# Kernel optimization log

Measured on AMD Instinct MI355X. Metric: run time of the kernel, lower is better.

## Reference

```python
import jax, jax.numpy as jnp
import numpy as np

DIM = 2048
N_HEADS = 16
N_KV_HEADS = 4
HEAD_DIM = DIM // N_HEADS  # 128
N_REP = N_HEADS // N_KV_HEADS
MAX_SEQ_LEN = 4096
SEQLEN = 4096


def setup_inputs() -> dict:
    key = jax.random.key(0)
    ks = jax.random.split(key, 6)
    x = jax.random.normal(ks[0], (1, SEQLEN, DIM), dtype=jnp.float32)
    # rotary frequencies, llama-style theta=10000
    inv_freq = 1.0 / (10000.0 ** (np.arange(0, HEAD_DIM, 2, dtype=np.float32) / HEAD_DIM))
    t = np.arange(SEQLEN, dtype=np.float32)
    ang = np.outer(t, inv_freq)  # [S, head_dim/2]
    freqs_cos = jnp.asarray(np.cos(ang))
    freqs_sin = jnp.asarray(np.sin(ang))
    # additive causal mask [S, S]
    mask = jnp.where(jnp.tril(jnp.ones((SEQLEN, SEQLEN), dtype=bool)), 0.0, -1e9).astype(jnp.float32)
    sc = 0.02
    wq = jax.random.normal(ks[1], (DIM, N_HEADS * HEAD_DIM), dtype=jnp.float32) * sc
    wk = jax.random.normal(ks[2], (DIM, N_KV_HEADS * HEAD_DIM), dtype=jnp.float32) * sc
    wv = jax.random.normal(ks[3], (DIM, N_KV_HEADS * HEAD_DIM), dtype=jnp.float32) * sc
    wo = jax.random.normal(ks[4], (N_HEADS * HEAD_DIM, DIM), dtype=jnp.float32) * sc
    return {"x": x, "start_pos": 0, "freqs_cos": freqs_cos, "freqs_sin": freqs_sin,
            "mask": mask, "wq": wq, "wk": wk, "wv": wv, "wo": wo}


def _rope(x, cos, sin):
    # x: [b, s, h, d]; cos/sin: [s, d/2]; consecutive pairs form complex numbers
    b, s, h, d = x.shape
    xr = x.astype(jnp.float32).reshape(b, s, h, d // 2, 2)
    x1, x2 = xr[..., 0], xr[..., 1]
    c = cos[None, :, None, :]
    sn = sin[None, :, None, :]
    o1 = x1 * c - x2 * sn
    o2 = x1 * sn + x2 * c
    return jnp.stack([o1, o2], axis=-1).reshape(b, s, h, d).astype(x.dtype)


def reference(x, start_pos, freqs_cos, freqs_sin, mask, wq, wk, wv, wo):
    bsz, seqlen, _ = x.shape
    xq = (x @ wq).reshape(bsz, seqlen, N_HEADS, HEAD_DIM)
    xk = (x @ wk).reshape(bsz, seqlen, N_KV_HEADS, HEAD_DIM)
    xv = (x @ wv).reshape(bsz, seqlen, N_KV_HEADS, HEAD_DIM)
    xq = _rope(xq, freqs_cos, freqs_sin)
    xk = _rope(xk, freqs_cos, freqs_sin)
    # KV-cache append (cache is zeros before this call)
    cache_k = jnp.zeros((1, MAX_SEQ_LEN, N_KV_HEADS, HEAD_DIM), dtype=xk.dtype)
    cache_v = jnp.zeros((1, MAX_SEQ_LEN, N_KV_HEADS, HEAD_DIM), dtype=xv.dtype)
    cache_k = jax.lax.dynamic_update_slice(cache_k, xk, (0, start_pos, 0, 0))
    cache_v = jax.lax.dynamic_update_slice(cache_v, xv, (0, start_pos, 0, 0))
    keys = cache_k[:bsz, : start_pos + seqlen]    # [b, T, kvh, d]
    values = cache_v[:bsz, : start_pos + seqlen]
    # GQA repeat to full head count
    keys = jnp.repeat(keys, N_REP, axis=2)
    values = jnp.repeat(values, N_REP, axis=2)
    scale = 1.0 / jnp.sqrt(jnp.float32(HEAD_DIM))
    scores = jnp.einsum('bshd,bthd->bhst', xq, keys) * scale  # [b, h, s, T]
    scores = scores + mask[None, None, :, :]
    probs = jax.nn.softmax(scores.astype(jnp.float32), axis=-1).astype(xq.dtype)
    out = jnp.einsum('bhst,bthd->bshd', probs, values).reshape(bsz, seqlen, -1)
    return out @ wo
```

## Files before the change

kernel.cpp:

```cpp
#include <hip/hip_runtime.h>
#include <hip/hip_bf16.h>
#include <stdint.h>

#define SEQ 4096
#define DIM 2048
#define NH 16
#define NKV 4
#define HD 128
#define KVLD 1024


using frag8 = __attribute__((ext_vector_type(8))) short;
using f32x4 = __attribute__((ext_vector_type(4))) float;

union VecU { ushort u[8]; uint4 v; };

__device__ __forceinline__ float bf2f(ushort u) {
    union { uint32_t u; float f; } v; v.u = ((uint32_t)u) << 16; return v.f;
}
__device__ __forceinline__ ushort f2bf(float f) {
    union { float f; uint32_t u; } v; v.f = f;
    uint32_t r = v.u + 0x7fffu + ((v.u >> 16) & 1u);
    return (ushort)(r >> 16);
}

__device__ __forceinline__ void glds16(const void* g, void* l) {
    __builtin_amdgcn_global_load_lds(
        (const __attribute__((address_space(1))) void*)g,
        (__attribute__((address_space(3))) void*)l, 16, 0, 0);
}

__global__ __launch_bounds__(256) void cvt_kernel(
    const float* __restrict__ src, ushort* __restrict__ dst)
{
    size_t i = ((size_t)blockIdx.x * 256 + threadIdx.x) * 8;
    float4 f0 = *(const float4*)&src[i];
    float4 f1 = *(const float4*)&src[i + 4];
    VecU t;
    t.u[0] = f2bf(f0.x); t.u[1] = f2bf(f0.y); t.u[2] = f2bf(f0.z); t.u[3] = f2bf(f0.w);
    t.u[4] = f2bf(f1.x); t.u[5] = f2bf(f1.y); t.u[6] = f2bf(f1.z); t.u[7] = f2bf(f1.w);
    *(uint4*)&dst[i] = t.v;
}

__global__ __launch_bounds__(256) void convT_kernel(
    const float* __restrict__ src, ushort* __restrict__ dst, int K, int N)
{
    __shared__ ushort T[32][36];
    int r  = threadIdx.x >> 3;
    int c4 = (threadIdx.x & 7) * 4;
    int bk = blockIdx.y * 32, bn = blockIdx.x * 32;
    float4 v = *(const float4*)&src[(size_t)(bk + r) * N + bn + c4];
    T[r][c4]     = f2bf(v.x); T[r][c4 + 1] = f2bf(v.y);
    T[r][c4 + 2] = f2bf(v.z); T[r][c4 + 3] = f2bf(v.w);
    __syncthreads();
    ushort4 o;
    o.x = T[c4][r]; o.y = T[c4 + 1][r]; o.z = T[c4 + 2][r]; o.w = T[c4 + 3][r];
    *(ushort4*)&dst[(size_t)(bn + r) * K + bk + c4] = o;
}

__global__ __launch_bounds__(256) void vtrans_kernel(
    const ushort* __restrict__ src, ushort* __restrict__ dst)
{
    __shared__ ushort T[32][36];
    int r  = threadIdx.x >> 3;
    int c4 = (threadIdx.x & 7) * 4;
    int bt = blockIdx.y * 32, bd = blockIdx.x * 32;
    ushort4 v = *(const ushort4*)&src[(size_t)(bt + r) * KVLD + 512 + bd + c4];
    T[r][c4] = v.x; T[r][c4 + 1] = v.y; T[r][c4 + 2] = v.z; T[r][c4 + 3] = v.w;
    __syncthreads();
    ushort4 o;
    o.x = T[c4][r]; o.y = T[c4 + 1][r]; o.z = T[c4 + 2][r]; o.w = T[c4 + 3][r];
    *(ushort4*)&dst[(size_t)(bd + r) * SEQ + bt + c4] = o;
}

template <int CF>
__global__ __launch_bounds__(256) void gemm_tn(
    const ushort* __restrict__ A, const ushort* __restrict__ BT,
    void* __restrict__ C, int M, int N, int K)
{
    __shared__ ushort As[128 * 32];
    __shared__ ushort Bs[128 * 32];

    const int tid  = threadIdx.x;
    const int lane = tid & 63;
    const int wave = tid >> 6;
    const int bm   = blockIdx.y * 128;
    const int bn   = blockIdx.x * 128;
    const int wm   = (wave >> 1) * 64;
    const int wn   = (wave & 1) * 64;
    const int quad = lane >> 4;
    const int t16  = lane & 15;
    const int kg   = quad ^ ((t16 >> 1) & 3);

    f32x4 acc[4][4] = {};

    for (int k0 = 0; k0 < K; k0 += 32) {
        #pragma unroll
        for (int it = 0; it < 2; ++it) {
            int gid = it * 256 + tid;
            int r   = gid >> 2;
            int cs  = (gid & 3) ^ ((gid >> 3) & 3);
            glds16(&A[(size_t)(bm + r) * K + k0 + cs * 8],
                   &As[(it * 256 + wave * 64) * 8]);
            glds16(&BT[(size_t)(bn + r) * K + k0 + cs * 8],
                   &Bs[(it * 256 + wave * 64) * 8]);
        }
        __syncthreads();

        frag8 af[4], bf[4];
        #pragma unroll
        for (int i = 0; i < 4; ++i)
            af[i] = *(const frag8*)&As[(wm + i * 16 + t16) * 32 + kg * 8];
        #pragma unroll
        for (int j = 0; j < 4; ++j)
            bf[j] = *(const frag8*)&Bs[(wn + j * 16 + t16) * 32 + kg * 8];
        #pragma unroll
        for (int i = 0; i < 4; ++i)
            #pragma unroll
            for (int j = 0; j < 4; ++j)
                acc[i][j] = __builtin_amdgcn_mfma_f32_16x16x32_bf16(
                    af[i], bf[j], acc[i][j], 0, 0, 0);
        __syncthreads();
    }

    #pragma unroll
    for (int i = 0; i < 4; ++i)
        #pragma unroll
        for (int j = 0; j < 4; ++j)
            #pragma unroll
            for (int r = 0; r < 4; ++r) {
                int row = bm + wm + i * 16 + quad * 4 + r;
                int col = bn + wn + j * 16 + t16;
                if (CF) ((float*)C)[(size_t)row * N + col] = acc[i][j][r];
                else    ((ushort*)C)[(size_t)row * N + col] = f2bf(acc[i][j][r]);
            }
}

__global__ __launch_bounds__(256) void gemm_qkv(
    const ushort* __restrict__ A, const ushort* __restrict__ BT,
    ushort* __restrict__ Cq, ushort* __restrict__ Ckv)
{
    const int K = DIM;
    __shared__ ushort As[128 * 32];
    __shared__ ushort Bs[128 * 32];

    const int tid  = threadIdx.x;
    const int lane = tid & 63;
    const int wave = tid >> 6;
    const int bm   = blockIdx.y * 128;
    const int bn   = blockIdx.x * 128;
    const int wm   = (wave >> 1) * 64;
    const int wn   = (wave & 1) * 64;
    const int quad = lane >> 4;
    const int t16  = lane & 15;
    const int kg   = quad ^ ((t16 >> 1) & 3);

    f32x4 acc[4][4] = {};

    for (int k0 = 0; k0 < K; k0 += 32) {
        #pragma unroll
        for (int it = 0; it < 2; ++it) {
            int gid = it * 256 + tid;
            int r   = gid >> 2;
            int cs  = (gid & 3) ^ ((gid >> 3) & 3);
            glds16(&A[(size_t)(bm + r) * K + k0 + cs * 8],
                   &As[(it * 256 + wave * 64) * 8]);
            glds16(&BT[(size_t)(bn + r) * K + k0 + cs * 8],
                   &Bs[(it * 256 + wave * 64) * 8]);
        }
        __syncthreads();

        frag8 af[4], bf[4];
        #pragma unroll
        for (int i = 0; i < 4; ++i)
            af[i] = *(const frag8*)&As[(wm + i * 16 + t16) * 32 + kg * 8];
        #pragma unroll
        for (int j = 0; j < 4; ++j)
            bf[j] = *(const frag8*)&Bs[(wn + j * 16 + t16) * 32 + kg * 8];
        #pragma unroll
        for (int i = 0; i < 4; ++i)
            #pragma unroll
            for (int j = 0; j < 4; ++j)
                acc[i][j] = __builtin_amdgcn_mfma_f32_16x16x32_bf16(
                    af[i], bf[j], acc[i][j], 0, 0, 0);
        __syncthreads();
    }

    ushort* C;
    int ldc, cb;
    if (bn < 2048) { C = Cq;  ldc = DIM;  cb = 0; }
    else           { C = Ckv; ldc = KVLD; cb = 2048; }

    #pragma unroll
    for (int i = 0; i < 4; ++i)
        #pragma unroll
        for (int j = 0; j < 4; ++j)
            #pragma unroll
            for (int r = 0; r < 4; ++r) {
                int row = bm + wm + i * 16 + quad * 4 + r;
                int col = bn + wn + j * 16 + t16;
                C[(size_t)row * ldc + (col - cb)] = f2bf(acc[i][j][r]);
            }
}

__global__ void rope_kernel(ushort* __restrict__ X, const float* __restrict__ Cos,
                            const float* __restrict__ Sin, int log2nh, int strideT,
                            float oscale)
{
    int idx = blockIdx.x * blockDim.x + threadIdx.x;
    int p = idx & 63;
    int h = (idx >> 6) & ((1 << log2nh) - 1);
    int t = idx >> (6 + log2nh);
    size_t base = (size_t)t * strideT + (size_t)h * 128 + 2 * p;
    ushort2 xv = *(ushort2*)&X[base];
    float x1 = bf2f(xv.x), x2 = bf2f(xv.y);
    float c = Cos[t * 64 + p], s = Sin[t * 64 + p];
    ushort2 ov;
    ov.x = f2bf((x1 * c - x2 * s) * oscale);
    ov.y = f2bf((x1 * s + x2 * c) * oscale);
    *(ushort2*)&X[base] = ov;
}

__global__ __launch_bounds__(256, 2) void attn_kernel(
    const ushort* __restrict__ Q, const ushort* __restrict__ Kb,
    const ushort* __restrict__ VT, ushort* __restrict__ O)
{
    __shared__ ushort Ks[64][136];
    __shared__ ushort Vt[128][72];
    __shared__ ushort Sp[4][32][72];

    const int tid  = threadIdx.x;
    const int lane = tid & 63;
    const int wave = tid >> 6;
    const int quad = lane >> 4;
    const int t16  = lane & 15;
    const int hp   = blockIdx.x;
    const int hA   = 2 * hp;
    const int hB   = 2 * hp + 1;
    const int kvh  = hp >> 1;

    frag8 vONE;
    #pragma unroll
    for (int i = 0; i < 8; ++i) vONE[i] = (short)0x3F80;

    const int qt = 63 - (int)blockIdx.y;
    const int q0 = qt * 64;
    const int qwave = q0 + wave * 16;
    const int qmaxw = qwave + 15;

    frag8 aQA[4], aQB[4];
    #pragma unroll
    for (int kk = 0; kk < 4; ++kk) {
        aQA[kk] = *(const frag8*)&Q[(size_t)(qwave + t16) * DIM + hA * HD + kk * 32 + quad * 8];
        aQB[kk] = *(const frag8*)&Q[(size_t)(qwave + t16) * DIM + hB * HD + kk * 32 + quad * 8];
    }

    f32x4 oA[8] = {}, oB[8] = {};
    f32x4 o9A = {0.f, 0.f, 0.f, 0.f};
    f32x4 o9B = {0.f, 0.f, 0.f, 0.f};
    float mA[4] = {0.f, 0.f, 0.f, 0.f};
    float mB[4] = {0.f, 0.f, 0.f, 0.f};

    for (int t0 = 0; t0 <= q0 + 63; t0 += 64) {
        #pragma unroll
        for (int it = 0; it < 4; ++it) {
            int idx = tid + it * 256;
            int tt  = idx >> 4;
            int c   = (idx & 15) * 8;
            *(uint4*)&Ks[tt][c] =
                *(const uint4*)&Kb[(size_t)(t0 + tt) * KVLD + kvh * HD + c];
        }
        #pragma unroll
        for (int it = 0; it < 4; ++it) {
            int idx = tid + it * 256;
            int d   = idx >> 3;
            int tq  = (idx & 7) * 8;
            *(uint4*)&Vt[d][tq] =
                *(const uint4*)&VT[(size_t)(kvh * HD + d) * SEQ + t0 + tq];
        }
        __syncthreads();

        const bool hi = (t0 + 32 <= qmaxw);

        f32x4 sA0 = {0.f,0.f,0.f,0.f}, sA1 = {0.f,0.f,0.f,0.f};
        f32x4 sA2 = {0.f,0.f,0.f,0.f}, sA3 = {0.f,0.f,0.f,0.f};
        f32x4 sB0 = {0.f,0.f,0.f,0.f}, sB1 = {0.f,0.f,0.f,0.f};
        f32x4 sB2 = {0.f,0.f,0.f,0.f}, sB3 = {0.f,0.f,0.f,0.f};

        __builtin_amdgcn_s_setprio(1);
        #pragma unroll
        for (int kk = 0; kk < 4; ++kk) {
            frag8 b0 = *(const frag8*)&Ks[2 * t16][kk * 32 + quad * 8];
            frag8 b1 = *(const frag8*)&Ks[2 * t16 + 1][kk * 32 + quad * 8];
            sA0 = __builtin_amdgcn_mfma_f32_16x16x32_bf16(aQA[kk], b0, sA0, 0, 0, 0);
            sB0 = __builtin_amdgcn_mfma_f32_16x16x32_bf16(aQB[kk], b0, sB0, 0, 0, 0);
            sA1 = __builtin_amdgcn_mfma_f32_16x16x32_bf16(aQA[kk], b1, sA1, 0, 0, 0);
            sB1 = __builtin_amdgcn_mfma_f32_16x16x32_bf16(aQB[kk], b1, sB1, 0, 0, 0);
        }
        if (hi) {
            #pragma unroll
            for (int kk = 0; kk < 4; ++kk) {
                frag8 b2 = *(const frag8*)&Ks[32 + 2 * t16][kk * 32 + quad * 8];
                frag8 b3 = *(const frag8*)&Ks[33 + 2 * t16][kk * 32 + quad * 8];
                sA2 = __builtin_amdgcn_mfma_f32_16x16x32_bf16(aQA[kk], b2, sA2, 0, 0, 0);
                sB2 = __builtin_amdgcn_mfma_f32_16x16x32_bf16(aQB[kk], b2, sB2, 0, 0, 0);
                sA3 = __builtin_amdgcn_mfma_f32_16x16x32_bf16(aQA[kk], b3, sA3, 0, 0, 0);
                sB3 = __builtin_amdgcn_mfma_f32_16x16x32_bf16(aQB[kk], b3, sB3, 0, 0, 0);
            }
        }
        __builtin_amdgcn_s_setprio(0);

        const bool mLo = (t0 + 31 > qwave);
        const bool mHi = (t0 + 63 > qwave);

        bool trig = false;
        #pragma unroll
        for (int r = 0; r < 4; ++r) {
            int q = qwave + quad * 4 + r;
            bool x0 = mLo && (t0 + 2 * t16 > q);
            bool x1 = mLo && (t0 + 2 * t16 + 1 > q);
            bool x2 = mHi && (t0 + 32 + 2 * t16 > q);
            bool x3 = mHi && (t0 + 33 + 2 * t16 > q);
            float vA0 = x0 ? -30000.f : sA0[r];
            float vA1 = x1 ? -30000.f : sA1[r];
            float vA2 = (hi && !x2) ? sA2[r] : -30000.f;
            float vA3 = (hi && !x3) ? sA3[r] : -30000.f;
            float vB0 = x0 ? -30000.f : sB0[r];
            float vB1 = x1 ? -30000.f : sB1[r];
            float vB2 = (hi && !x2) ? sB2[r] : -30000.f;
            float vB3 = (hi && !x3) ? sB3[r] : -30000.f;
            float lmA = fmaxf(fmaxf(vA0, vA1), fmaxf(vA2, vA3));
            float lmB = fmaxf(fmaxf(vB0, vB1), fmaxf(vB2, vB3));
            trig |= (lmA > mA[r] + 8.f) | (lmB > mB[r] + 8.f);
            float eA0 = __expf(vA0 - mA[r]);
            float eA1 = __expf(vA1 - mA[r]);
            float eB0 = __expf(vB0 - mB[r]);
            float eB1 = __expf(vB1 - mB[r]);
            *(uint*)&Sp[wave][quad * 4 + r][2 * t16] =
                (uint)f2bf(eA0) | ((uint)f2bf(eA1) << 16);
            *(uint*)&Sp[wave][16 + quad * 4 + r][2 * t16] =
                (uint)f2bf(eB0) | ((uint)f2bf(eB1) << 16);
            if (hi) {
                float eA2 = __expf(vA2 - mA[r]);
                float eA3 = __expf(vA3 - mA[r]);
                float eB2 = __expf(vB2 - mB[r]);
                float eB3 = __expf(vB3 - mB[r]);
                *(uint*)&Sp[wave][quad * 4 + r][32 + 2 * t16] =
                    (uint)f2bf(eA2) | ((uint)f2bf(eA3) << 16);
                *(uint*)&Sp[wave][16 + quad * 4 + r][32 + 2 * t16] =
                    (uint)f2bf(eB2) | ((uint)f2bf(eB3) << 16);
            }
        }

        if (__any(trig)) {
            #pragma unroll
            for (int r = 0; r < 4; ++r) {
                int q = qwave + quad * 4 + r;
                bool x0 = mLo && (t0 + 2 * t16 > q);
                bool x1 = mLo && (t0 + 2 * t16 + 1 > q);
                bool x2 = mHi && (t0 + 32 + 2 * t16 > q);
                bool x3 = mHi && (t0 + 33 + 2 * t16 > q);
                float vA0 = x0 ? -30000.f : sA0[r];
                float vA1 = x1 ? -30000.f : sA1[r];
                float vA2 = (hi && !x2) ? sA2[r] : -30000.f;
                float vA3 = (hi && !x3) ? sA3[r] : -30000.f;
                float vB0 = x0 ? -30000.f : sB0[r];
                float vB1 = x1 ? -30000.f : sB1[r];
                float vB2 = (hi && !x2) ? sB2[r] : -30000.f;
                float vB3 = (hi && !x3) ? sB3[r] : -30000.f;
                float rmA = fmaxf(fmaxf(vA0, vA1), fmaxf(vA2, vA3));
                float rmB = fmaxf(fmaxf(vB0, vB1), fmaxf(vB2, vB3));
                rmA = fmaxf(rmA, __shfl_xor(rmA, 1));
                rmA = fmaxf(rmA, __shfl_xor(rmA, 2));
                rmA = fmaxf(rmA, __shfl_xor(rmA, 4));
                rmA = fmaxf(rmA, __shfl_xor(rmA, 8));
                rmB = fmaxf(rmB, __shfl_xor(rmB, 1));
                rmB = fmaxf(rmB, __shfl_xor(rmB, 2));
                rmB = fmaxf(rmB, __shfl_xor(rmB, 4));
                rmB = fmaxf(rmB, __shfl_xor(rmB, 8));
                float mnA = fmaxf(mA[r], rmA);
                float mnB = fmaxf(mB[r], rmB);
                float alA = __expf(mA[r] - mnA);
                float alB = __expf(mB[r] - mnB);
                #pragma unroll
                for (int j = 0; j < 8; ++j) { oA[j][r] *= alA; oB[j][r] *= alB; }
                o9A[r] *= alA; o9B[r] *= alB;
                mA[r] = mnA; mB[r] = mnB;
                float eA0 = __expf(vA0 - mnA);
                float eA1 = __expf(vA1 - mnA);
                float eB0 = __expf(vB0 - mnB);
                float eB1 = __expf(vB1 - mnB);
                *(uint*)&Sp[wave][quad * 4 + r][2 * t16] =
                    (uint)f2bf(eA0) | ((uint)f2bf(eA1) << 16);
                *(uint*)&Sp[wave][16 + quad * 4 + r][2 * t16] =
                    (uint)f2bf(eB0) | ((uint)f2bf(eB1) << 16);
                if (hi) {
                    float eA2 = __expf(vA2 - mnA);
                    float eA3 = __expf(vA3 - mnA);
                    float eB2 = __expf(vB2 - mnB);
                    float eB3 = __expf(vB3 - mnB);
                    *(uint*)&Sp[wave][quad * 4 + r][32 + 2 * t16] =
                        (uint)f2bf(eA2) | ((uint)f2bf(eA3) << 16);
                    *(uint*)&Sp[wave][16 + quad * 4 + r][32 + 2 * t16] =
                        (uint)f2bf(eB2) | ((uint)f2bf(eB3) << 16);
                }
            }
        }

        frag8 aPA0 = *(const frag8*)&Sp[wave][t16][quad * 8];
        frag8 aPB0 = *(const frag8*)&Sp[wave][16 + t16][quad * 8];
        __builtin_amdgcn_s_setprio(1);
        #pragma unroll
        for (int j = 0; j < 8; ++j) {
            frag8 bV = *(const frag8*)&Vt[j * 16 + t16][quad * 8];
            oA[j] = __builtin_amdgcn_mfma_f32_16x16x32_bf16(aPA0, bV, oA[j], 0, 0, 0);
            oB[j] = __builtin_amdgcn_mfma_f32_16x16x32_bf16(aPB0, bV, oB[j], 0, 0, 0);
        }
        o9A = __builtin_amdgcn_mfma_f32_16x16x32_bf16(aPA0, vONE, o9A, 0, 0, 0);
        o9B = __builtin_amdgcn_mfma_f32_16x16x32_bf16(aPB0, vONE, o9B, 0, 0, 0);
        if (hi) {
            frag8 aPA1 = *(const frag8*)&Sp[wave][t16][32 + quad * 8];
            frag8 aPB1 = *(const frag8*)&Sp[wave][16 + t16][32 + quad * 8];
            #pragma unroll
            for (int j = 0; j < 8; ++j) {
                frag8 bV = *(const frag8*)&Vt[j * 16 + t16][32 + quad * 8];
                oA[j] = __builtin_amdgcn_mfma_f32_16x16x32_bf16(aPA1, bV, oA[j], 0, 0, 0);
                oB[j] = __builtin_amdgcn_mfma_f32_16x16x32_bf16(aPB1, bV, oB[j], 0, 0, 0);
            }
            o9A = __builtin_amdgcn_mfma_f32_16x16x32_bf16(aPA1, vONE, o9A, 0, 0, 0);
            o9B = __builtin_amdgcn_mfma_f32_16x16x32_bf16(aPB1, vONE, o9B, 0, 0, 0);
        }
        __builtin_amdgcn_s_setprio(0);
        __syncthreads();
    }

    #pragma unroll
    for (int r = 0; r < 4; ++r) {
        float invA = 1.f / fmaxf(o9A[r], 1e-20f);
        float invB = 1.f / fmaxf(o9B[r], 1e-20f);
        int row = qwave + quad * 4 + r;
        #pragma unroll
        for (int j = 0; j < 8; ++j) {
            O[(size_t)row * DIM + hA * HD + j * 16 + t16] = f2bf(oA[j][r] * invA);
            O[(size_t)row * DIM + hB * HD + j * 16 + t16] = f2bf(oB[j][r] * invB);
        }
    }
}

extern "C" void kernel_launch(void* const* d_in, const int* in_sizes, int n_in,
                              void* d_out, int out_size, void* d_ws, size_t ws_size,
                              hipStream_t stream)
{
    const float* x  = (const float*)d_in[0];
    const float* fc = (const float*)d_in[2];
    const float* fs = (const float*)d_in[3];
    const float* wq = (const float*)d_in[5];
    const float* wk = (const float*)d_in[6];
    const float* wv = (const float*)d_in[7];
    const float* wo = (const float*)d_in[8];

    ushort* Qb  = (ushort*)d_ws;
    ushort* KVb = Qb + (size_t)SEQ * DIM;
    ushort* Ab  = KVb + (size_t)SEQ * KVLD;
    ushort* WqT = Ab;
    ushort* KVT = Ab + (size_t)DIM * DIM;
    ushort* WoT = KVb;

    ushort* Xb = (ushort*)d_out;
    ushort* VT = Xb + (size_t)SEQ * DIM;

    dim3 blk(256);

    cvt_kernel<<<(SEQ * DIM) / 2048, blk, 0, stream>>>(x, Xb);
    convT_kernel<<<dim3(DIM / 32, DIM / 32), blk, 0, stream>>>(wq, WqT, DIM, DIM);
    convT_kernel<<<dim3(512 / 32, DIM / 32), blk, 0, stream>>>(wk, KVT, DIM, 512);
    convT_kernel<<<dim3(512 / 32, DIM / 32), blk, 0, stream>>>(
        wv, KVT + (size_t)512 * DIM, DIM, 512);

    gemm_qkv<<<dim3(3072 / 128, SEQ / 128), blk, 0, stream>>>(Xb, Ab, Qb, KVb);

    rope_kernel<<<(SEQ * NH * 64) / 256, blk, 0, stream>>>(
        Qb, fc, fs, 4, DIM, 0.08838834764831845f);
    rope_kernel<<<(SEQ * NKV * 64) / 256, blk, 0, stream>>>(
        KVb, fc, fs, 2, KVLD, 1.0f);

    vtrans_kernel<<<dim3(512 / 32, SEQ / 32), blk, 0, stream>>>(KVb, VT);

    attn_kernel<<<dim3(NH / 2, 64), blk, 0, stream>>>(Qb, KVb, VT, Ab);

    convT_kernel<<<dim3(DIM / 32, DIM / 32), blk, 0, stream>>>(wo, WoT, DIM, DIM);
    gemm_tn<1><<<dim3(DIM / 128, SEQ / 128), blk, 0, stream>>>(Ab, WoT, d_out, SEQ, DIM, DIM);
}
```

Before: 450.9 us.

## Split long causal attention query tiles across two blocks and merge partials

The 32 longest query tiles (rows 2048+) now have their key range split in half across two blocks. Each block writes unnormalized partial outputs plus its row sum and max to scratch, and a new combine kernel rescales and merges the halves. The goal is to balance the causal triangle's uneven work and give the GPU more blocks. The launch-bounds occupancy hint is also raised from 2 to 3. In exchange it adds an extra kernel, extra global traffic for the partials, and a bf16 rounding of the unnormalized partials.

```diff
diff --git a/kernel.cpp b/kernel.cpp
--- a/kernel.cpp
+++ b/kernel.cpp
@@ -221,9 +221,10 @@
     *(ushort2*)&X[base] = ov;
 }
 
-__global__ __launch_bounds__(256, 2) void attn_kernel(
+__global__ __launch_bounds__(256, 3) void attn_kernel(
     const ushort* __restrict__ Q, const ushort* __restrict__ Kb,
-    const ushort* __restrict__ VT, ushort* __restrict__ O)
+    const ushort* __restrict__ VT, ushort* __restrict__ Oab,
+    ushort* __restrict__ Oev, float2* __restrict__ lmE, float2* __restrict__ lmO)
 {
     __shared__ ushort Ks[64][136];
     __shared__ ushort Vt[128][72];
@@ -243,10 +244,16 @@
     #pragma unroll
     for (int i = 0; i < 8; ++i) vONE[i] = (short)0x3F80;
 
-    const int qt = 63 - (int)blockIdx.y;
+    const int by = (int)blockIdx.y;
+    int qt, c, split;
+    if (by < 64) { split = 1; qt = 63 - (by >> 1); c = by & 1; }
+    else         { split = 0; qt = 95 - by;        c = 0;      }
+    const int n  = qt + 1;
     const int q0 = qt * 64;
     const int qwave = q0 + wave * 16;
     const int qmaxw = qwave + 15;
+    const int tstart = (split && c) ? (n / 2) * 64 : 0;
+    const int tend   = (split && !c) ? (n / 2) * 64 : n * 64;
 
     frag8 aQA[4], aQB[4];
     #pragma unroll
@@ -261,14 +268,14 @@
     float mA[4] = {0.f, 0.f, 0.f, 0.f};
     float mB[4] = {0.f, 0.f, 0.f, 0.f};
 
-    for (int t0 = 0; t0 <= q0 + 63; t0 += 64) {
+    for (int t0 = tstart; t0 < tend; t0 += 64) {
         #pragma unroll
         for (int it = 0; it < 4; ++it) {
             int idx = tid + it * 256;
             int tt  = idx >> 4;
-            int c   = (idx & 15) * 8;
-            *(uint4*)&Ks[tt][c] =
-                *(const uint4*)&Kb[(size_t)(t0 + tt) * KVLD + kvh * HD + c];
+            int cc  = (idx & 15) * 8;
+            *(uint4*)&Ks[tt][cc] =
+                *(const uint4*)&Kb[(size_t)(t0 + tt) * KVLD + kvh * HD + cc];
         }
         #pragma unroll
         for (int it = 0; it < 4; ++it) {
@@ -434,17 +441,59 @@
         __syncthreads();
     }
 
+    if (split) {
+        ushort* dst = c ? Oab : Oev;
+        float2* lm  = c ? lmO : lmE;
+        #pragma unroll
+        for (int r = 0; r < 4; ++r) {
+            int row = qwave + quad * 4 + r;
+            if (t16 == 0) {
+                lm[(size_t)(row - 2048) * NH + hA] = make_float2(o9A[r], mA[r]);
+                lm[(size_t)(row - 2048) * NH + hB] = make_float2(o9B[r], mB[r]);
+            }
+            #pragma unroll
+            for (int j = 0; j < 8; ++j) {
+                dst[(size_t)row * DIM + hA * HD + j * 16 + t16] = f2bf(oA[j][r]);
+                dst[(size_t)row * DIM + hB * HD + j * 16 + t16] = f2bf(oB[j][r]);
+            }
+        }
+    } else {
+        #pragma unroll
+        for (int r = 0; r < 4; ++r) {
+            float invA = 1.f / fmaxf(o9A[r], 1e-20f);
+            float invB = 1.f / fmaxf(o9B[r], 1e-20f);
+            int row = qwave + quad * 4 + r;
+            #pragma unroll
+            for (int j = 0; j < 8; ++j) {
+                Oab[(size_t)row * DIM + hA * HD + j * 16 + t16] = f2bf(oA[j][r] * invA);
+                Oab[(size_t)row * DIM + hB * HD + j * 16 + t16] = f2bf(oB[j][r] * invB);
+            }
+        }
+    }
+}
+
+__global__ __launch_bounds__(256) void combine_kernel(
+    const ushort* __restrict__ oE, const ushort* __restrict__ oO,
+    const float2* __restrict__ lmE, const float2* __restrict__ lmO,
+    ushort* __restrict__ out)
+{
+    size_t e = (size_t)(SEQ / 2) * DIM + ((size_t)blockIdx.x * 256 + threadIdx.x) * 8;
+    int row = (int)(e >> 11);
+    int h   = (int)((e >> 7) & 15);
+    float2 LE = lmE[(size_t)(row - 2048) * NH + h];
+    float2 LO = lmO[(size_t)(row - 2048) * NH + h];
+    float ms = fmaxf(LE.y, LO.y);
+    float aE = __expf(LE.y - ms);
+    float aO = __expf(LO.y - ms);
+    float inv = 1.f / fmaxf(LE.x * aE + LO.x * aO, 1e-20f);
+    aE *= inv; aO *= inv;
+    VecU uE, uO, uR;
+    uE.v = *(const uint4*)&oE[e];
+    uO.v = *(const uint4*)&oO[e];
     #pragma unroll
-    for (int r = 0; r < 4; ++r) {
-        float invA = 1.f / fmaxf(o9A[r], 1e-20f);
-        float invB = 1.f / fmaxf(o9B[r], 1e-20f);
-        int row = qwave + quad * 4 + r;
-        #pragma unroll
-        for (int j = 0; j < 8; ++j) {
-            O[(size_t)row * DIM + hA * HD + j * 16 + t16] = f2bf(oA[j][r] * invA);
-            O[(size_t)row * DIM + hB * HD + j * 16 + t16] = f2bf(oB[j][r] * invB);
-        }
-    }
+    for (int j = 0; j < 8; ++j)
+        uR.u[j] = f2bf(bf2f(uE.u[j]) * aE + bf2f(uO.u[j]) * aO);
+    *(uint4*)&out[e] = uR.v;
 }
 
 extern "C" void kernel_launch(void* const* d_in, const int* in_sizes, int n_in,
@@ -468,6 +517,8 @@
 
     ushort* Xb = (ushort*)d_out;
     ushort* VT = Xb + (size_t)SEQ * DIM;
+    float2* lmE = (float2*)(VT + (size_t)512 * SEQ);
+    float2* lmO = lmE + (size_t)(SEQ / 2) * NH;
 
     dim3 blk(256);
 
@@ -486,7 +537,11 @@
 
     vtrans_kernel<<<dim3(512 / 32, SEQ / 32), blk, 0, stream>>>(KVb, VT);
 
-    attn_kernel<<<dim3(NH / 2, 64), blk, 0, stream>>>(Qb, KVb, VT, Ab);
+    attn_kernel<<<dim3(NH / 2, 96), blk, 0, stream>>>(
+        Qb, KVb, VT, Ab, Xb, lmE, lmO);
+
+    combine_kernel<<<(SEQ / 2) * DIM / 2048, blk, 0, stream>>>(
+        Xb, Ab, lmE, lmO, Ab);
 
     convT_kernel<<<dim3(DIM / 32, DIM / 32), blk, 0, stream>>>(wo, WoT, DIM, DIM);
     gemm_tn<1><<<dim3(DIM / 128, SEQ / 128), blk, 0, stream>>>(Ab, WoT, d_out, SEQ, DIM, DIM);
```

Measured after the change: 579.5 us. 1.29x slower.
